# Kernel optimization log

Hardware: AMD Instinct MI355X
Metric: run time of the kernel (lower is better)

Reference implementation:

```python
import jax, jax.numpy as jnp
import numpy as np

N_NODES = 50000; N_INTRA = 800000; N_INTER = 400000; N_IEDGE = 600000
N_GRAPHS = 128; F_IN = 54; DIM = 128; N_GNN = 3; DIM_MLP = 128
DEV_VDW_COEFF = 0.2; EPS_LO = 0.0178; EPS_HI = 0.2
VDW_N_SHORT = 10.0; VDW_N_LONG = 6.0
RANGE_LO = 0.5; RANGE_HI = 5.0
HBOND_CUT = (-0.7, 0.0); METAL_CUT = (-0.7, 0.0); HYDRO_CUT = (0.5, 1.5)


def _lin(key, fi, fo):
    return jax.random.normal(key, (fi, fo), jnp.float32) / np.float32(np.sqrt(fi))


def setup_inputs():
    key = jax.random.key(0)
    ks = iter(jax.random.split(key, 48))
    nk = lambda: next(ks)
    inp = {}
    inp['x'] = jax.random.normal(nk(), (N_NODES, F_IN), jnp.float32)
    inp['pos'] = jax.random.uniform(nk(), (N_NODES, 3), jnp.float32, 0.0, 20.0)
    inp['vdw_radii'] = jax.random.uniform(nk(), (N_NODES,), jnp.float32, 1.0, 2.0)
    inp['rotor'] = jax.random.randint(nk(), (N_GRAPHS, 1), 0, 20).astype(jnp.float32)
    inp['edge_index'] = jax.random.randint(nk(), (2, N_INTRA), 0, N_NODES)
    inp['edge_index_c'] = jax.random.randint(nk(), (2, N_INTER), 0, N_NODES)
    inp['edge_index_i'] = jax.random.randint(nk(), (2, N_IEDGE), 0, N_NODES)
    inp['batch'] = jnp.sort(jax.random.randint(nk(), (N_NODES,), 0, N_GRAPHS))
    for name, p in (('is_metal', 0.02), ('is_h_donor', 0.15), ('is_h_acceptor', 0.2), ('is_hydrophobic', 0.4)):
        inp[name] = jax.random.bernoulli(nk(), p, (N_NODES,))
    inp['embed_W'] = _lin(nk(), F_IN, DIM)
    inp['gat_W'] = jax.random.normal(nk(), (N_GNN, DIM, DIM), jnp.float32) / np.float32(np.sqrt(DIM))
    inp['gat_Wb'] = jnp.zeros((N_GNN, DIM), jnp.float32)
    inp['gat_A'] = 0.1 * jax.random.normal(nk(), (N_GNN, DIM, DIM), jnp.float32) / np.float32(np.sqrt(DIM))
    inp['gat_gate_w'] = jax.random.normal(nk(), (N_GNN, 2 * DIM, 1), jnp.float32) / np.float32(np.sqrt(2 * DIM))
    inp['gat_gate_b'] = jnp.zeros((N_GNN, 1), jnp.float32)
    inp['inter_W'] = jax.random.normal(nk(), (N_GNN, DIM, DIM), jnp.float32) / np.float32(np.sqrt(DIM))
    inp['inter_Wb'] = jnp.zeros((N_GNN, DIM), jnp.float32)
    inp['inter_gate_w'] = jax.random.normal(nk(), (N_GNN, 2 * DIM, 1), jnp.float32) / np.float32(np.sqrt(2 * DIM))
    inp['inter_gate_b'] = jnp.zeros((N_GNN, 1), jnp.float32)
    inp['eps_w1'] = _lin(nk(), 2 * DIM, DIM_MLP); inp['eps_b1'] = jnp.zeros((DIM_MLP,), jnp.float32)
    inp['eps_w2'] = _lin(nk(), DIM_MLP, 1); inp['eps_b2'] = jnp.zeros((1,), jnp.float32)
    inp['dvdw_w1'] = _lin(nk(), 2 * DIM, DIM_MLP); inp['dvdw_b1'] = jnp.zeros((DIM_MLP,), jnp.float32)
    inp['dvdw_w2'] = _lin(nk(), DIM_MLP, 1); inp['dvdw_b2'] = jnp.zeros((1,), jnp.float32)
    inp['hbond_coeff'] = jnp.array([1.0], jnp.float32)
    inp['hydrophobic_coeff'] = jnp.array([0.5], jnp.float32)
    inp['rotor_coeff'] = jnp.array([0.5], jnp.float32)
    return inp


def _gated_gat(x, src, dst, W, Wb, A, gw, gb):
    n = x.shape[0]
    h = x @ W + Wb                                   # [N, D]
    logits = jnp.sum((h @ A)[dst] * h[src], axis=-1)  # per-edge attention logit
    mx = jax.ops.segment_max(logits, dst, num_segments=n)
    mx = jnp.where(jnp.isfinite(mx), mx, 0.0)
    ex = jnp.exp(logits - mx[dst])
    den = jax.ops.segment_sum(ex, dst, num_segments=n)
    alpha = ex / (den[dst] + 1e-16)                  # segment softmax over incoming edges
    h_prime = jax.nn.relu(jax.ops.segment_sum(alpha[:, None] * h[src], dst, num_segments=n))
    z = jax.nn.sigmoid(jnp.concatenate([x, h_prime], -1) @ gw + gb)
    return z * x + (1.0 - z) * h_prime


def _interaction(x, src, dst, W, Wb, gw, gb):
    n = x.shape[0]
    m = jax.ops.segment_sum(jax.nn.relu(x[src] @ W + Wb), dst, num_segments=n)
    z = jax.nn.sigmoid(jnp.concatenate([x, m], -1) @ gw + gb)
    return z * x + (1.0 - z) * m


def _lj(D, R, eps, n_short, n_long):
    dr = jnp.maximum(D / R, 0.5)  # numerical clamp mirroring PIGNet's distance clamp
    n = jnp.where(dr < 1.0, n_short, n_long)
    return eps * (dr ** (-2.0 * n) - 2.0 * dr ** (-n))


def _linear_potential(D, R, minima, c_short, c_long):
    frac = jnp.clip(((D - R) - c_long) / (c_short - c_long), 0.0, 1.0)
    return minima * frac


def _forward(x, pos, vdw_radii, rotor, embed_W, gat_W, gat_Wb, gat_A, gat_gate_w, gat_gate_b,
             inter_W, inter_Wb, inter_gate_w, inter_gate_b,
             eps_w1, eps_b1, eps_w2, eps_b2, dvdw_w1, dvdw_b1, dvdw_w2, dvdw_b2,
             hbond_coeff, hydrophobic_coeff, rotor_coeff,
             edge_index, edge_index_c, edge_index_i, batch,
             is_metal, is_h_donor, is_h_acceptor, is_hydrophobic):
    h = x @ embed_W
    for l in range(N_GNN):
        h = _gated_gat(h, edge_index[0], edge_index[1], gat_W[l], gat_Wb[l], gat_A[l], gat_gate_w[l], gat_gate_b[l])
    for l in range(N_GNN):
        h = _interaction(h, edge_index_c[0], edge_index_c[1], inter_W[l], inter_Wb[l], inter_gate_w[l], inter_gate_b[l])
    i, j = edge_index_i[0], edge_index_i[1]
    diff = pos[i] - pos[j]
    D = jnp.sqrt(jnp.sum(diff * diff, axis=-1) + 1e-10)           # [E]
    rmask = ((D >= RANGE_LO) & (D <= RANGE_HI)).astype(h.dtype)
    x_cat = jnp.concatenate([h[i], h[j]], axis=-1)                # [E, 2*DIM]
    dvdw = jnp.tanh(jax.nn.relu(x_cat @ dvdw_w1 + dvdw_b1) @ dvdw_w2 + dvdw_b2)[:, 0]
    dvdw = dvdw * DEV_VDW_COEFF * rmask
    R = vdw_radii[i] + vdw_radii[j] + dvdw
    eps = jax.nn.sigmoid(jax.nn.relu(x_cat @ eps_w1 + eps_b1) @ eps_w2 + eps_b2)[:, 0]
    eps = eps * (EPS_HI - EPS_LO) + EPS_LO
    min_hb = -hbond_coeff ** 2
    min_hp = -hydrophobic_coeff ** 2
    e = jnp.stack([
        _lj(D, R, eps, VDW_N_SHORT, VDW_N_LONG),
        _linear_potential(D, R, min_hb, *HBOND_CUT),
        _linear_potential(D, R, min_hb, *METAL_CUT),
        _linear_potential(D, R, min_hp, *HYDRO_CUT),
    ])                                                            # [4, E]
    no_metal = ~(is_metal[i] | is_metal[j])
    masks = jnp.stack([
        no_metal,
        ((is_h_donor[i] & is_h_acceptor[j]) | (is_h_acceptor[i] & is_h_donor[j])) & no_metal,
        (is_metal[i] & is_h_acceptor[j]) | (is_h_acceptor[i] & is_metal[j]),
        is_hydrophobic[i] & is_hydrophobic[j] & no_metal,
    ]).astype(e.dtype)
    e = e * masks * rmask
    energies = jax.ops.segment_sum(e.T, batch[i], num_segments=N_GRAPHS)  # [G, 4]
    penalty = 1.0 + rotor_coeff ** 2 * rotor                               # [G, 1]
    return energies / penalty, dvdw


def reference(x, pos, vdw_radii, rotor, edge_index, edge_index_c, edge_index_i, batch,
              is_metal, is_h_donor, is_h_acceptor, is_hydrophobic,
              embed_W, gat_W, gat_Wb, gat_A, gat_gate_w, gat_gate_b,
              inter_W, inter_Wb, inter_gate_w, inter_gate_b,
              eps_w1, eps_b1, eps_w2, eps_b2, dvdw_w1, dvdw_b1, dvdw_w2, dvdw_b2,
              hbond_coeff, hydrophobic_coeff, rotor_coeff):
    return _forward(x, pos, vdw_radii, rotor, embed_W, gat_W, gat_Wb, gat_A, gat_gate_w, gat_gate_b,
                    inter_W, inter_Wb, inter_gate_w, inter_gate_b,
                    eps_w1, eps_b1, eps_w2, eps_b2, dvdw_w1, dvdw_b1, dvdw_w2, dvdw_b2,
                    hbond_coeff, hydrophobic_coeff, rotor_coeff,
                    edge_index, edge_index_c, edge_index_i, batch,
                    is_metal, is_h_donor, is_h_acceptor, is_hydrophobic)
```

## Files before the change

### kernel.cpp

```cpp
#include <hip/hip_runtime.h>
#include <math.h>

#define NN 50000
#define EA 800000
#define EC 400000
#define EIN 600000
#define NG 128
#define FIN 54

#define DEV_VDW 0.2f
#define EPS_LO_ 0.0178f
#define EPS_HI_ 0.2f

typedef unsigned int uint;
typedef unsigned short ushort;
typedef unsigned long long ull;
typedef __attribute__((ext_vector_type(8))) short bf16x8;
typedef __attribute__((ext_vector_type(4))) float f32x4;

__device__ __forceinline__ ushort f2bf(float f){
  uint x = __float_as_uint(f);
  uint r = x + 0x7fffu + ((x >> 16) & 1u);
  return (ushort)(r >> 16);
}
__device__ __forceinline__ uint f2bf2(float a, float b){
  return (uint)f2bf(a) | ((uint)f2bf(b) << 16);
}
__device__ __forceinline__ void decode8(uint4 u, float* f){
  f[0] = __uint_as_float(u.x << 16); f[1] = __uint_as_float(u.x & 0xffff0000u);
  f[2] = __uint_as_float(u.y << 16); f[3] = __uint_as_float(u.y & 0xffff0000u);
  f[4] = __uint_as_float(u.z << 16); f[5] = __uint_as_float(u.z & 0xffff0000u);
  f[6] = __uint_as_float(u.w << 16); f[7] = __uint_as_float(u.w & 0xffff0000u);
}

__global__ void k_rank(const int* __restrict__ dstA, const int* __restrict__ dstC,
                       const int* __restrict__ dstI,
                       int* __restrict__ cntA, int* __restrict__ cntC, int* __restrict__ cntI,
                       int* __restrict__ rnkA, int* __restrict__ rnkC, int* __restrict__ rnkI){
  int b = blockIdx.x;
  const int* dst; int* cnt; int* rnk; int E; int bid; int nb;
  if (b < 1024){ dst = dstA; cnt = cntA; rnk = rnkA; E = EA;  bid = b;        nb = 1024; }
  else if (b < 1536){ dst = dstC; cnt = cntC; rnk = rnkC; E = EC;  bid = b - 1024; nb = 512; }
  else { dst = dstI; cnt = cntI; rnk = rnkI; E = EIN; bid = b - 1536; nb = 1024; }
  for (int i = bid * 256 + threadIdx.x; i < E; i += nb * 256)
    rnk[i] = atomicAdd(&cnt[dst[i]], 1);
}

__global__ void k_scan3(const int* __restrict__ cntA, int* __restrict__ offA,
                        const int* __restrict__ cntC, int* __restrict__ offC,
                        const int* __restrict__ cntI, int* __restrict__ offI){
  const int* cnt = (blockIdx.x == 0) ? cntA : (blockIdx.x == 1) ? cntC : cntI;
  int* off = (blockIdx.x == 0) ? offA : (blockIdx.x == 1) ? offC : offI;
  int n = NN;
  __shared__ int wsums[16];
  __shared__ int run_s;
  int tid = threadIdx.x;
  int lane = tid & 63, w = tid >> 6;
  if (tid == 0) run_s = 0;
  __syncthreads();
  for (int base = 0; base < n; base += 1024){
    int run = run_s;
    int i = base + tid;
    int v = (i < n) ? cnt[i] : 0;
    int s = v;
    #pragma unroll
    for (int o = 1; o < 64; o <<= 1){ int t = __shfl_up(s, o, 64); if (lane >= o) s += t; }
    if (lane == 63) wsums[w] = s;
    __syncthreads();
    if (w == 0 && lane < 16){
      int t = wsums[lane];
      #pragma unroll
      for (int o = 1; o < 16; o <<= 1){ int u = __shfl_up(t, o, 64); if (lane >= o) t += u; }
      wsums[lane] = t;
    }
    __syncthreads();
    int woff = (w == 0) ? 0 : wsums[w - 1];
    int excl = run + woff + (s - v);
    if (i < n) off[i] = excl;
    int tot = wsums[15];
    __syncthreads();
    if (tid == 0) run_s = run + tot;
    __syncthreads();
  }
  if (threadIdx.x == 0) off[n] = run_s;
}

__global__ void k_place(const int* __restrict__ eiA, const int* __restrict__ eiC,
                        const int* __restrict__ eiI,
                        const int* __restrict__ offA, const int* __restrict__ rnkA, int* __restrict__ srcA,
                        const int* __restrict__ offC, const int* __restrict__ rnkC, int* __restrict__ srcC,
                        const int* __restrict__ offI, const int* __restrict__ rnkI, ull* __restrict__ jeI){
  int b = blockIdx.x;
  if (b < 1024){
    for (int i = b * 256 + threadIdx.x; i < EA; i += 1024 * 256){
      int d = eiA[EA + i];
      __builtin_nontemporal_store(eiA[i], &srcA[offA[d] + rnkA[i]]);
    }
  } else if (b < 1536){
    int bid = b - 1024;
    for (int i = bid * 256 + threadIdx.x; i < EC; i += 512 * 256){
      int d = eiC[EC + i];
      __builtin_nontemporal_store(eiC[i], &srcC[offC[d] + rnkC[i]]);
    }
  } else {
    int bid = b - 1536;
    for (int i = bid * 256 + threadIdx.x; i < EIN; i += 1024 * 256){
      int key = eiI[i];
      ull v = ((ull)(uint)i << 32) | (uint)eiI[EIN + i];
      __builtin_nontemporal_store(v, &jeI[offI[key] + rnkI[i]]);
    }
  }
}

__global__ void k_nodeinfo(const float* __restrict__ POS, const float* __restrict__ RAD,
                           const int* __restrict__ Mmet, const int* __restrict__ Mdon,
                           const int* __restrict__ Macc, const int* __restrict__ Mhyd,
                           const int* __restrict__ BATCH,
                           float4* __restrict__ PRAD, uint* __restrict__ MB){
  int n = blockIdx.x * 256 + threadIdx.x;
  if (n < NN){
    PRAD[n] = make_float4(POS[3*n], POS[3*n+1], POS[3*n+2], RAD[n]);
    uint m = (Mmet[n] ? 1u : 0u) | (Mdon[n] ? 2u : 0u) | (Macc[n] ? 4u : 0u) |
             (Mhyd[n] ? 8u : 0u) | ((uint)BATCH[n] << 8);
    MB[n] = m;
  }
}

__global__ __launch_bounds__(256) void k_prepw(const float* __restrict__ gatW, const float* __restrict__ gatA,
                        const float* __restrict__ intW, const float* __restrict__ dw1,
                        const float* __restrict__ ew1,
                        const float* __restrict__ gatWb, const float* __restrict__ intWb,
                        const float* __restrict__ db1, const float* __restrict__ eb1,
                        uint* __restrict__ Wt, float* __restrict__ BIASALL){
  __shared__ ushort L[128 * 132];
  int m = blockIdx.x;
  int tid = threadIdx.x;
  if (m == 13){
    for (int idx = tid; idx < 13 * 128; idx += 256){
      int slot = idx >> 7, c = idx & 127;
      if (slot >= 3 && slot < 6) continue;
      float v = 0.f;
      if (slot < 3) v = gatWb[slot * 128 + c];
      else if (slot < 9) v = intWb[(slot - 6) * 128 + c];
      else if (slot == 9) v = db1[c];
      else if (slot == 11) v = eb1[c];
      BIASALL[idx] = v;
    }
    return;
  }
  if (m >= 3 && m < 6){
    int l = m - 3;
    const float* Wf  = gatW + l * 16384;
    const float* Af  = gatA + l * 16384;
    const float* Wbf = gatWb + l * 128;
    for (int idx = tid; idx < 16384; idx += 256){
      int k = idx >> 7, n = idx & 127;
      L[k * 132 + n] = f2bf(Af[idx]);
    }
    __syncthreads();
    int r = tid >> 1, ch = tid & 1;
    float accv[64];
    #pragma unroll
    for (int c = 0; c < 64; ++c) accv[c] = 0.f;
    float accb = 0.f;
    int bc = tid & 127;
    for (int mm = 0; mm < 128; ++mm){
      float wv = Wf[r * 128 + mm];
      const uint* Lr32 = (const uint*)&L[mm * 132 + ch * 64];
      #pragma unroll
      for (int c2 = 0; c2 < 32; ++c2){
        uint u = Lr32[c2];
        accv[2 * c2]     += wv * __uint_as_float(u << 16);
        accv[2 * c2 + 1] += wv * __uint_as_float(u & 0xffff0000u);
      }
      accb += Wbf[mm] * __uint_as_float((uint)L[mm * 132 + bc] << 16);
    }
    __syncthreads();
    #pragma unroll
    for (int c = 0; c < 64; ++c) L[r * 132 + ch * 64 + c] = f2bf(accv[c]);
    if (tid < 128) BIASALL[(3 + l) * 128 + tid] = accb;
    __syncthreads();
    int n = tid & 127, half = tid >> 7;
    uint* outp = Wt + (size_t)m * 8192 + n * 64 + half * 32;
    #pragma unroll
    for (int kk2 = 0; kk2 < 32; ++kk2){
      int k = half * 64 + 2 * kk2;
      uint u = (uint)L[k * 132 + n] | ((uint)L[(k + 1) * 132 + n] << 16);
      outp[kk2] = u;
    }
    return;
  }
  const float* src = (m < 3)  ? gatW + m * 16384 :
                     (m < 9)  ? intW + (m - 6) * 16384 :
                     (m < 11) ? dw1 + (m - 9) * 16384 :
                                ew1 + (m - 11) * 16384;
  for (int idx = tid; idx < 16384; idx += 256){
    int k = idx >> 7, n = idx & 127;
    L[k * 132 + n] = f2bf(src[idx]);
  }
  __syncthreads();
  int n = tid & 127, half = tid >> 7;
  uint* outp = Wt + (size_t)m * 8192 + n * 64 + half * 32;
  #pragma unroll
  for (int kk2 = 0; kk2 < 32; ++kk2){
    int k = half * 64 + 2 * kk2;
    uint u = (uint)L[k * 132 + n] | ((uint)L[(k + 1) * 132 + n] << 16);
    outp[kk2] = u;
  }
}

__global__ void k_embed(const float* __restrict__ X, const float* __restrict__ W,
                        uint* __restrict__ Hh){
  __shared__ float Wls[FIN * 128];
  int tid = threadIdx.x;
  for (int i = tid; i < FIN * 128; i += 128) Wls[i] = W[i];
  __syncthreads();
  for (int row = blockIdx.x; row < NN; row += gridDim.x){
    const float* xr = X + row * FIN;
    float acc = 0.f;
    #pragma unroll
    for (int k = 0; k < FIN; ++k) acc += xr[k] * Wls[k * 128 + tid];
    ((ushort*)Hh)[(size_t)row * 128 + tid] = f2bf(acc);
  }
}

template<bool RELU>
__global__ __launch_bounds__(256) void k_gemm_mfma(const uint* __restrict__ Ah,
        const uint* __restrict__ Bt0, size_t strideB,
        const float* __restrict__ bias0, size_t strideBias,
        uint* __restrict__ C0, size_t strideC, int N){
  const uint* Bt = Bt0 + (size_t)blockIdx.y * strideB;
  const float* bias = bias0 + (size_t)blockIdx.y * strideBias;
  uint* Cout = C0 + (size_t)blockIdx.y * strideC;
  int tid = threadIdx.x;
  int lane = tid & 63;
  int wv = tid >> 6;
  int row0 = blockIdx.x * 128 + wv * 32;
  int l15 = lane & 15, lg = lane >> 4;
  int ra0 = row0 + l15, ra1 = row0 + 16 + l15;
  const uint* pa0 = Ah + (size_t)(ra0 < N ? ra0 : 0) * 64 + lg * 4;
  const uint* pa1 = Ah + (size_t)(ra1 < N ? ra1 : 0) * 64 + lg * 4;
  const uint* pb  = Bt + (size_t)l15 * 64 + lg * 4;
  f32x4 acc[2][8] = {};
  #pragma unroll
  for (int c = 0; c < 4; ++c){
    bf16x8 a0 = *(const bf16x8*)(pa0 + c * 16);
    bf16x8 a1 = *(const bf16x8*)(pa1 + c * 16);
    #pragma unroll
    for (int ct = 0; ct < 8; ++ct){
      bf16x8 b = *(const bf16x8*)(pb + ct * 1024 + c * 16);
      acc[0][ct] = __builtin_amdgcn_mfma_f32_16x16x32_bf16(a0, b, acc[0][ct], 0, 0, 0);
      acc[1][ct] = __builtin_amdgcn_mfma_f32_16x16x32_bf16(a1, b, acc[1][ct], 0, 0, 0);
    }
  }
  #pragma unroll
  for (int ct = 0; ct < 8; ++ct){
    int col = ct * 16 + l15;
    float bv = bias[col];
    #pragma unroll
    for (int rt = 0; rt < 2; ++rt){
      int rbase = row0 + rt * 16 + lg * 4;
      f32x4 a4 = acc[rt][ct];
      #pragma unroll
      for (int r = 0; r < 4; ++r){
        int row = rbase + r;
        if (row < N){
          float t = a4[r] + bv;
          if (RELU) t = fmaxf(t, 0.f);
          ((ushort*)Cout)[(size_t)row * 128 + col] = f2bf(t);
        }
      }
    }
  }
}

__global__ __launch_bounds__(256) void k_gat(uint* __restrict__ Hh,
                      const uint* __restrict__ HWh, const uint* __restrict__ HAh,
                      const int* __restrict__ off, const int* __restrict__ srcs,
                      const float* __restrict__ GW, const float* __restrict__ GB){
  int tid = threadIdx.x;
  int sub = tid & 15;
  int n = blockIdx.x * 16 + (tid >> 4);
  if (n >= NN) return;
  uint4 au = *(const uint4*)(HAh + (size_t)n * 64 + sub * 4);
  float a[8]; decode8(au, a);
  int e0 = off[n], deg = off[n + 1] - e0;
  float m = -INFINITY, den = 0.f;
  float acc[8] = {};
  uint4 w0v = {}, w1v = {}, w2v = {};
  if (deg > 0) w0v = *(const uint4*)(HWh + (size_t)srcs[e0] * 64 + sub * 4);
  if (deg > 1) w1v = *(const uint4*)(HWh + (size_t)srcs[e0 + 1] * 64 + sub * 4);
  if (deg > 2) w2v = *(const uint4*)(HWh + (size_t)srcs[e0 + 2] * 64 + sub * 4);
  for (int t = 0; t < deg; ++t){
    uint4 wn = {};
    if (t + 3 < deg) wn = *(const uint4*)(HWh + (size_t)srcs[e0 + t + 3] * 64 + sub * 4);
    float w[8]; decode8(w0v, w);
    float p = a[0]*w[0] + a[1]*w[1] + a[2]*w[2] + a[3]*w[3]
            + a[4]*w[4] + a[5]*w[5] + a[6]*w[6] + a[7]*w[7];
    #pragma unroll
    for (int o = 8; o; o >>= 1) p += __shfl_xor(p, o, 64);
    float mn = fmaxf(m, p);
    float cf = __expf(m - mn);
    float ex = __expf(p - mn);
    den = den * cf + ex;
    #pragma unroll
    for (int q = 0; q < 8; ++q) acc[q] = acc[q] * cf + ex * w[q];
    m = mn;
    w0v = w1v; w1v = w2v; w2v = wn;
  }
  float inv = 1.f / (den + 1e-16f);
  float hp[8];
  #pragma unroll
  for (int q = 0; q < 8; ++q) hp[q] = fmaxf(acc[q] * inv, 0.f);
  uint4 xu = *(const uint4*)(Hh + (size_t)n * 64 + sub * 4);
  float x[8]; decode8(xu, x);
  float gx[8], gh[8];
  *(float4*)&gx[0] = *(const float4*)(GW + sub * 8);
  *(float4*)&gx[4] = *(const float4*)(GW + sub * 8 + 4);
  *(float4*)&gh[0] = *(const float4*)(GW + 128 + sub * 8);
  *(float4*)&gh[4] = *(const float4*)(GW + 128 + sub * 8 + 4);
  float g = 0.f;
  #pragma unroll
  for (int q = 0; q < 8; ++q) g += x[q] * gx[q] + hp[q] * gh[q];
  #pragma unroll
  for (int o = 8; o; o >>= 1) g += __shfl_xor(g, o, 64);
  g += GB[0];
  float z = 1.f / (1.f + __expf(-g));
  #pragma unroll
  for (int q = 0; q < 8; ++q) x[q] = z * x[q] + (1.f - z) * hp[q];
  uint4 hw;
  hw.x = f2bf2(x[0], x[1]); hw.y = f2bf2(x[2], x[3]);
  hw.z = f2bf2(x[4], x[5]); hw.w = f2bf2(x[6], x[7]);
  *(uint4*)(Hh + (size_t)n * 64 + sub * 4) = hw;
}

__global__ __launch_bounds__(256) void k_inter(uint* __restrict__ Hh,
                        const uint* __restrict__ Th,
                        const int* __restrict__ off, const int* __restrict__ srcs,
                        const float* __restrict__ GW, const float* __restrict__ GB){
  int tid = threadIdx.x;
  int sub = tid & 15;
  int n = blockIdx.x * 16 + (tid >> 4);
  if (n >= NN) return;
  int e0 = off[n], deg = off[n + 1] - e0;
  float acc[8] = {};
  uint4 w0v = {}, w1v = {}, w2v = {};
  if (deg > 0) w0v = *(const uint4*)(Th + (size_t)srcs[e0] * 64 + sub * 4);
  if (deg > 1) w1v = *(const uint4*)(Th + (size_t)srcs[e0 + 1] * 64 + sub * 4);
  if (deg > 2) w2v = *(const uint4*)(Th + (size_t)srcs[e0 + 2] * 64 + sub * 4);
  for (int t = 0; t < deg; ++t){
    uint4 wn = {};
    if (t + 3 < deg) wn = *(const uint4*)(Th + (size_t)srcs[e0 + t + 3] * 64 + sub * 4);
    float w[8]; decode8(w0v, w);
    #pragma unroll
    for (int q = 0; q < 8; ++q) acc[q] += w[q];
    w0v = w1v; w1v = w2v; w2v = wn;
  }
  uint4 xu = *(const uint4*)(Hh + (size_t)n * 64 + sub * 4);
  float x[8]; decode8(xu, x);
  float gx[8], gh[8];
  *(float4*)&gx[0] = *(const float4*)(GW + sub * 8);
  *(float4*)&gx[4] = *(const float4*)(GW + sub * 8 + 4);
  *(float4*)&gh[0] = *(const float4*)(GW + 128 + sub * 8);
  *(float4*)&gh[4] = *(const float4*)(GW + 128 + sub * 8 + 4);
  float g = 0.f;
  #pragma unroll
  for (int q = 0; q < 8; ++q) g += x[q] * gx[q] + acc[q] * gh[q];
  #pragma unroll
  for (int o = 8; o; o >>= 1) g += __shfl_xor(g, o, 64);
  g += GB[0];
  float z = 1.f / (1.f + __expf(-g));
  #pragma unroll
  for (int q = 0; q < 8; ++q) x[q] = z * x[q] + (1.f - z) * acc[q];
  uint4 hw;
  hw.x = f2bf2(x[0], x[1]); hw.y = f2bf2(x[2], x[3]);
  hw.z = f2bf2(x[4], x[5]); hw.w = f2bf2(x[6], x[7]);
  *(uint4*)(Hh + (size_t)n * 64 + sub * 4) = hw;
}

__global__ __launch_bounds__(256) void k_edges(
    const int* __restrict__ offI, const ull* __restrict__ jeI,
    const float4* __restrict__ PRAD, const uint* __restrict__ MB,
    const uint* __restrict__ Pd, const uint* __restrict__ Qd,
    const uint* __restrict__ Pe, const uint* __restrict__ Qe,
    const float* __restrict__ w2d, const float* __restrict__ b2d,
    const float* __restrict__ w2e, const float* __restrict__ b2e,
    const float* __restrict__ hbc, const float* __restrict__ hpc,
    float* __restrict__ geng, float* __restrict__ outdv){
  int tid = threadIdx.x;
  int sub = tid & 15;
  int n = blockIdx.x * 16 + (tid >> 4);
  if (n >= NN) return;
  int e0 = offI[n], deg = offI[n + 1] - e0;
  if (deg == 0) return;
  float wdv[8], wev[8];
  *(float4*)&wdv[0] = *(const float4*)(w2d + sub * 8);
  *(float4*)&wdv[4] = *(const float4*)(w2d + sub * 8 + 4);
  *(float4*)&wev[0] = *(const float4*)(w2e + sub * 8);
  *(float4*)&wev[4] = *(const float4*)(w2e + sub * 8 + 4);
  float bd = b2d[0], be = b2e[0];
  float minhb = -hbc[0] * hbc[0], minhp = -hpc[0] * hpc[0];
  uint4 pdu = *(const uint4*)(Pd + (size_t)n * 64 + sub * 4);
  uint4 peu = *(const uint4*)(Pe + (size_t)n * 64 + sub * 4);
  float pdf[8], pef[8];
  decode8(pdu, pdf); decode8(peu, pef);
  float4 pri = PRAD[n];
  uint mbi = MB[n];
  float E0 = 0.f, E1 = 0.f, E2 = 0.f, E3 = 0.f;

  ull je0 = jeI[e0];
  int j0 = (int)(uint)je0;
  uint4 qd0 = *(const uint4*)(Qd + (size_t)j0 * 64 + sub * 4);
  uint4 qe0 = *(const uint4*)(Qe + (size_t)j0 * 64 + sub * 4);
  float4 prj0 = PRAD[j0];
  uint mbj0 = MB[j0];

  for (int t = 0; t < deg; ++t){
    ull je1 = 0; uint4 qd1 = {}, qe1 = {}; float4 prj1 = {}; uint mbj1 = 0;
    if (t + 1 < deg){
      je1 = jeI[e0 + t + 1];
      int j1 = (int)(uint)je1;
      qd1 = *(const uint4*)(Qd + (size_t)j1 * 64 + sub * 4);
      qe1 = *(const uint4*)(Qe + (size_t)j1 * 64 + sub * 4);
      prj1 = PRAD[j1]; mbj1 = MB[j1];
    }
    float qdf[8], qef[8];
    decode8(qd0, qdf); decode8(qe0, qef);
    float sd = 0.f, se = 0.f;
    #pragma unroll
    for (int q = 0; q < 8; ++q){
      sd += fmaxf(pdf[q] + qdf[q], 0.f) * wdv[q];
      se += fmaxf(pef[q] + qef[q], 0.f) * wev[q];
    }
    #pragma unroll
    for (int o = 8; o; o >>= 1){
      sd += __shfl_xor(sd, o, 64);
      se += __shfl_xor(se, o, 64);
    }
    sd += bd; se += be;
    float dx = pri.x - prj0.x, dy = pri.y - prj0.y, dz = pri.z - prj0.z;
    float D = sqrtf(dx * dx + dy * dy + dz * dz + 1e-10f);
    float rmask = (D >= 0.5f && D <= 5.0f) ? 1.f : 0.f;
    float ex2 = __expf(2.f * fminf(sd, 15.f));
    float th = __fdividef(ex2 - 1.f, ex2 + 1.f);
    float dvdw = th * DEV_VDW * rmask;
    float eps = __fdividef(1.f, 1.f + __expf(-se)) * (EPS_HI_ - EPS_LO_) + EPS_LO_;
    float R = pri.w + prj0.w + dvdw;
    float dr = fmaxf(__fdividef(D, R), 0.5f);
    float nn2 = (dr < 1.f) ? 10.f : 6.f;
    float tp = __expf(-nn2 * __logf(dr));
    float ev = eps * (tp * tp - 2.f * tp);
    float dmr = D - R;
    float f1 = fminf(fmaxf(dmr * (-1.f / 0.7f), 0.f), 1.f);
    float f3 = fminf(fmaxf(1.5f - dmr, 0.f), 1.f);
    bool metI = mbi & 1, metJ = mbj0 & 1;
    bool donI = mbi & 2, donJ = mbj0 & 2;
    bool accI = mbi & 4, accJ = mbj0 & 4;
    bool hyI  = mbi & 8, hyJ  = mbj0 & 8;
    bool nm = !(metI || metJ);
    if (sub == 0) __builtin_nontemporal_store(dvdw, &outdv[(int)(je0 >> 32)]);
    E0 += nm ? ev * rmask : 0.f;
    E1 += (((donI && accJ) || (accI && donJ)) && nm) ? minhb * f1 * rmask : 0.f;
    E2 += ((metI && accJ) || (accI && metJ)) ? minhb * f1 * rmask : 0.f;
    E3 += (hyI && hyJ && nm) ? minhp * f3 * rmask : 0.f;
    je0 = je1; qd0 = qd1; qe0 = qe1; prj0 = prj1; mbj0 = mbj1;
  }
  if (sub == 0){
    float* part = geng + (size_t)(blockIdx.x & 7) * (NG * 4);
    int g = (int)(mbi >> 8) * 4;
    atomicAdd(&part[g + 0], E0);
    atomicAdd(&part[g + 1], E1);
    atomicAdd(&part[g + 2], E2);
    atomicAdd(&part[g + 3], E3);
  }
}

__global__ void k_final(const float* __restrict__ geng, const float* __restrict__ rotor,
                        const float* __restrict__ rc, float* __restrict__ out){
  int t = blockIdx.x * blockDim.x + threadIdx.x;
  if (t < NG * 4){
    int g = t >> 2;
    float s = 0.f;
    #pragma unroll
    for (int p = 0; p < 8; ++p) s += geng[p * NG * 4 + t];
    float pen = 1.f + rc[0] * rc[0] * rotor[g];
    out[t] = s / pen;
  }
}

extern "C" void kernel_launch(void* const* d_in, const int* in_sizes, int n_in,
                              void* d_out, int out_size, void* d_ws, size_t ws_size,
                              hipStream_t stream){
  (void)in_sizes; (void)n_in; (void)out_size; (void)ws_size;
  const float* X    = (const float*)d_in[0];
  const float* POS  = (const float*)d_in[1];
  const float* RAD  = (const float*)d_in[2];
  const float* ROT  = (const float*)d_in[3];
  const int* EIa    = (const int*)d_in[4];
  const int* EIc    = (const int*)d_in[5];
  const int* EIi    = (const int*)d_in[6];
  const int* BATCH  = (const int*)d_in[7];
  const int* Mmet = (const int*)d_in[8];
  const int* Mdon = (const int*)d_in[9];
  const int* Macc = (const int*)d_in[10];
  const int* Mhyd = (const int*)d_in[11];
  const float* embW  = (const float*)d_in[12];
  const float* gatW  = (const float*)d_in[13];
  const float* gatWb = (const float*)d_in[14];
  const float* gatA  = (const float*)d_in[15];
  const float* gatGw = (const float*)d_in[16];
  const float* gatGb = (const float*)d_in[17];
  const float* intW  = (const float*)d_in[18];
  const float* intWb = (const float*)d_in[19];
  const float* intGw = (const float*)d_in[20];
  const float* intGb = (const float*)d_in[21];
  const float* ew1 = (const float*)d_in[22];
  const float* eb1 = (const float*)d_in[23];
  const float* ew2 = (const float*)d_in[24];
  const float* eb2 = (const float*)d_in[25];
  const float* dw1 = (const float*)d_in[26];
  const float* db1 = (const float*)d_in[27];
  const float* dw2 = (const float*)d_in[28];
  const float* db2 = (const float*)d_in[29];
  const float* hbc = (const float*)d_in[30];
  const float* hpc = (const float*)d_in[31];
  const float* rcc = (const float*)d_in[32];
  float* out = (float*)d_out;

  char* w = (char*)d_ws;
  uint* Hh   = (uint*)w;  w += (size_t)NN * 64 * 4;
  uint* BAh  = (uint*)w;  w += (size_t)NN * 64 * 4;
  uint* BBh  = (uint*)w;  w += (size_t)NN * 64 * 4;
  uint* Peh  = (uint*)w;  w += (size_t)NN * 64 * 4;
  uint* Qeh  = (uint*)w;  w += (size_t)NN * 64 * 4;
  uint* WT   = (uint*)w;  w += (size_t)13 * 8192 * 4;
  float* BIASALL = (float*)w; w += (size_t)13 * 128 * 4;
  float4* PRAD = (float4*)w; w += (size_t)NN * 16;
  uint* MBb  = (uint*)w;  w += (size_t)NN * 4;
  float* GENG = (float*)w; w += (size_t)8 * 512 * 4;
  int* cntA = (int*)w; w += (size_t)NN * 4;
  int* offA = (int*)w; w += (size_t)(NN + 1) * 4;
  int* srcA = (int*)w; w += (size_t)EA * 4;
  int* rnkA = (int*)w; w += (size_t)EA * 4;
  int* cntC = (int*)w; w += (size_t)NN * 4;
  int* offC = (int*)w; w += (size_t)(NN + 1) * 4;
  int* srcC = (int*)w; w += (size_t)EC * 4;
  int* rnkC = (int*)w; w += (size_t)EC * 4;
  int* cntI = (int*)w; w += (size_t)NN * 4;
  int* offI = (int*)w; w += (size_t)(NN + 1) * 4;
  int* rnkI = (int*)w; w += (size_t)EIN * 4;
  ull* jeI  = (ull*)w; w += (size_t)EIN * 8;
  uint* Th  = BAh;
  uint* Pdh = BAh;
  uint* Qdh = BBh;

  hipMemsetAsync(cntA, 0, (size_t)NN * 4, stream);
  hipMemsetAsync(cntC, 0, (size_t)NN * 4, stream);
  hipMemsetAsync(cntI, 0, (size_t)NN * 4, stream);
  hipMemsetAsync(GENG, 0, (size_t)8 * 512 * 4, stream);

  k_rank<<<2560, 256, 0, stream>>>(EIa + EA, EIc + EC, EIi, cntA, cntC, cntI, rnkA, rnkC, rnkI);
  k_scan3<<<3, 1024, 0, stream>>>(cntA, offA, cntC, offC, cntI, offI);
  k_place<<<2560, 256, 0, stream>>>(EIa, EIc, EIi, offA, rnkA, srcA, offC, rnkC, srcC, offI, rnkI, jeI);

  k_prepw<<<14, 256, 0, stream>>>(gatW, gatA, intW, dw1, ew1, gatWb, intWb, db1, eb1, WT, BIASALL);
  k_nodeinfo<<<(NN + 255) / 256, 256, 0, stream>>>(POS, RAD, Mmet, Mdon, Macc, Mhyd, BATCH, PRAD, MBb);
  k_embed<<<2048, 128, 0, stream>>>(X, embW, Hh);

  int gg = (NN + 127) / 128;
  int nodeGrid = (NN + 15) / 16;
  for (int l = 0; l < 3; ++l){
    k_gemm_mfma<false><<<dim3(gg, 2), 256, 0, stream>>>(Hh, WT + (size_t)l * 8192, (size_t)3 * 8192,
                                                        BIASALL + l * 128, (size_t)3 * 128,
                                                        BAh, (size_t)NN * 64, NN);
    k_gat<<<nodeGrid, 256, 0, stream>>>(Hh, BAh, BBh, offA, srcA, gatGw + l * 256, gatGb + l);
  }
  for (int l = 0; l < 3; ++l){
    k_gemm_mfma<true><<<dim3(gg, 1), 256, 0, stream>>>(Hh, WT + (size_t)(6 + l) * 8192, 0,
                                                       BIASALL + (6 + l) * 128, 0, Th, 0, NN);
    k_inter<<<nodeGrid, 256, 0, stream>>>(Hh, Th, offC, srcC, intGw + l * 256, intGb + l);
  }
  k_gemm_mfma<false><<<dim3(gg, 4), 256, 0, stream>>>(Hh, WT + (size_t)9 * 8192, (size_t)8192,
                                                      BIASALL + 9 * 128, (size_t)128,
                                                      BAh, (size_t)NN * 64, NN);

  k_edges<<<nodeGrid, 256, 0, stream>>>(offI, jeI, PRAD, MBb, Pdh, Qdh, Peh, Qeh,
                                        dw2, db2, ew2, eb2, hbc, hpc,
                                        GENG, out + 512);
  k_final<<<2, 256, 0, stream>>>(GENG, ROT, rcc, out);
}
```

Before: 889.0 us.

## Use atomic-cursor CSR placement, fuse setup kernels, balance edge work evenly

Edge bucketing now counts without storing ranks and takes slots from an atomic cursor copied from the scan, which removes the rank arrays. Weight prep, node info and the embedding are merged into one launch, and the four memsets become one. The online softmax in the GAT kernel uses a single exponential per edge instead of two. The interaction-edge kernel splits edges evenly across groups instead of one group per node, and flushes per-graph partial sums whenever the graph changes. The cost is extra gathers of the i-side rows per edge and more atomics, and slot order within a node is no longer deterministic.

```diff
diff --git a/kernel.cpp b/kernel.cpp
--- a/kernel.cpp
+++ b/kernel.cpp
@@ -33,24 +33,23 @@
   f[6] = __uint_as_float(u.w << 16); f[7] = __uint_as_float(u.w & 0xffff0000u);
 }
 
-__global__ void k_rank(const int* __restrict__ dstA, const int* __restrict__ dstC,
-                       const int* __restrict__ dstI,
-                       int* __restrict__ cntA, int* __restrict__ cntC, int* __restrict__ cntI,
-                       int* __restrict__ rnkA, int* __restrict__ rnkC, int* __restrict__ rnkI){
+__global__ void k_count(const int* __restrict__ dstA, const int* __restrict__ dstC,
+                        const int* __restrict__ dstI,
+                        int* __restrict__ cntA, int* __restrict__ cntC, int* __restrict__ cntI){
   int b = blockIdx.x;
-  const int* dst; int* cnt; int* rnk; int E; int bid; int nb;
-  if (b < 1024){ dst = dstA; cnt = cntA; rnk = rnkA; E = EA;  bid = b;        nb = 1024; }
-  else if (b < 1536){ dst = dstC; cnt = cntC; rnk = rnkC; E = EC;  bid = b - 1024; nb = 512; }
-  else { dst = dstI; cnt = cntI; rnk = rnkI; E = EIN; bid = b - 1536; nb = 1024; }
-  for (int i = bid * 256 + threadIdx.x; i < E; i += nb * 256)
-    rnk[i] = atomicAdd(&cnt[dst[i]], 1);
-}
-
-__global__ void k_scan3(const int* __restrict__ cntA, int* __restrict__ offA,
-                        const int* __restrict__ cntC, int* __restrict__ offC,
-                        const int* __restrict__ cntI, int* __restrict__ offI){
+  const int* dst; int* cnt; int E; int bid; int nb;
+  if (b < 1024){ dst = dstA; cnt = cntA; E = EA;  bid = b;        nb = 1024; }
+  else if (b < 1536){ dst = dstC; cnt = cntC; E = EC;  bid = b - 1024; nb = 512; }
+  else { dst = dstI; cnt = cntI; E = EIN; bid = b - 1536; nb = 1024; }
+  for (int i = bid * 256 + threadIdx.x; i < E; i += nb * 256) atomicAdd(&cnt[dst[i]], 1);
+}
+
+__global__ void k_scan3(const int* __restrict__ cntA, int* __restrict__ offA, int* __restrict__ curA,
+                        const int* __restrict__ cntC, int* __restrict__ offC, int* __restrict__ curC,
+                        const int* __restrict__ cntI, int* __restrict__ offI, int* __restrict__ curI){
   const int* cnt = (blockIdx.x == 0) ? cntA : (blockIdx.x == 1) ? cntC : cntI;
   int* off = (blockIdx.x == 0) ? offA : (blockIdx.x == 1) ? offC : offI;
+  int* cur = (blockIdx.x == 0) ? curA : (blockIdx.x == 1) ? curC : curI;
   int n = NN;
   __shared__ int wsums[16];
   __shared__ int run_s;
@@ -76,7 +75,7 @@
     __syncthreads();
     int woff = (w == 0) ? 0 : wsums[w - 1];
     int excl = run + woff + (s - v);
-    if (i < n) off[i] = excl;
+    if (i < n){ off[i] = excl; cur[i] = excl; }
     int tot = wsums[15];
     __syncthreads();
     if (tid == 0) run_s = run + tot;
@@ -87,54 +86,78 @@
 
 __global__ void k_place(const int* __restrict__ eiA, const int* __restrict__ eiC,
                         const int* __restrict__ eiI,
-                        const int* __restrict__ offA, const int* __restrict__ rnkA, int* __restrict__ srcA,
-                        const int* __restrict__ offC, const int* __restrict__ rnkC, int* __restrict__ srcC,
-                        const int* __restrict__ offI, const int* __restrict__ rnkI, ull* __restrict__ jeI){
+                        int* __restrict__ curA, int* __restrict__ srcA,
+                        int* __restrict__ curC, int* __restrict__ srcC,
+                        int* __restrict__ curI, ull* __restrict__ jeI, int* __restrict__ iI){
   int b = blockIdx.x;
   if (b < 1024){
     for (int i = b * 256 + threadIdx.x; i < EA; i += 1024 * 256){
       int d = eiA[EA + i];
-      __builtin_nontemporal_store(eiA[i], &srcA[offA[d] + rnkA[i]]);
+      int slot = atomicAdd(&curA[d], 1);
+      __builtin_nontemporal_store(eiA[i], &srcA[slot]);
     }
   } else if (b < 1536){
     int bid = b - 1024;
     for (int i = bid * 256 + threadIdx.x; i < EC; i += 512 * 256){
       int d = eiC[EC + i];
-      __builtin_nontemporal_store(eiC[i], &srcC[offC[d] + rnkC[i]]);
+      int slot = atomicAdd(&curC[d], 1);
+      __builtin_nontemporal_store(eiC[i], &srcC[slot]);
     }
   } else {
     int bid = b - 1536;
     for (int i = bid * 256 + threadIdx.x; i < EIN; i += 1024 * 256){
       int key = eiI[i];
+      int slot = atomicAdd(&curI[key], 1);
       ull v = ((ull)(uint)i << 32) | (uint)eiI[EIN + i];
-      __builtin_nontemporal_store(v, &jeI[offI[key] + rnkI[i]]);
-    }
-  }
-}
-
-__global__ void k_nodeinfo(const float* __restrict__ POS, const float* __restrict__ RAD,
-                           const int* __restrict__ Mmet, const int* __restrict__ Mdon,
-                           const int* __restrict__ Macc, const int* __restrict__ Mhyd,
-                           const int* __restrict__ BATCH,
-                           float4* __restrict__ PRAD, uint* __restrict__ MB){
-  int n = blockIdx.x * 256 + threadIdx.x;
-  if (n < NN){
-    PRAD[n] = make_float4(POS[3*n], POS[3*n+1], POS[3*n+2], RAD[n]);
-    uint m = (Mmet[n] ? 1u : 0u) | (Mdon[n] ? 2u : 0u) | (Macc[n] ? 4u : 0u) |
-             (Mhyd[n] ? 8u : 0u) | ((uint)BATCH[n] << 8);
-    MB[n] = m;
-  }
-}
-
-__global__ __launch_bounds__(256) void k_prepw(const float* __restrict__ gatW, const float* __restrict__ gatA,
+      __builtin_nontemporal_store(v, &jeI[slot]);
+      __builtin_nontemporal_store(key, &iI[slot]);
+    }
+  }
+}
+
+__global__ __launch_bounds__(256) void k_misc(
+                        const float* __restrict__ gatW, const float* __restrict__ gatA,
                         const float* __restrict__ intW, const float* __restrict__ dw1,
                         const float* __restrict__ ew1,
                         const float* __restrict__ gatWb, const float* __restrict__ intWb,
                         const float* __restrict__ db1, const float* __restrict__ eb1,
-                        uint* __restrict__ Wt, float* __restrict__ BIASALL){
-  __shared__ ushort L[128 * 132];
-  int m = blockIdx.x;
+                        uint* __restrict__ Wt, float* __restrict__ BIASALL,
+                        const float* __restrict__ POS, const float* __restrict__ RAD,
+                        const int* __restrict__ Mmet, const int* __restrict__ Mdon,
+                        const int* __restrict__ Macc, const int* __restrict__ Mhyd,
+                        const int* __restrict__ BATCH,
+                        float4* __restrict__ PRAD, uint* __restrict__ MB,
+                        const float* __restrict__ X, const float* __restrict__ embW,
+                        uint* __restrict__ Hh){
+  __shared__ char SMEM[33792];
+  int b = blockIdx.x;
   int tid = threadIdx.x;
+  if (b >= 210){
+    float* Wls = (float*)SMEM;
+    for (int i = tid; i < FIN * 128; i += 256) Wls[i] = embW[i];
+    __syncthreads();
+    int col = tid & 127, rh = tid >> 7;
+    for (int row = (b - 210) * 2 + rh; row < NN; row += 4096){
+      const float* xr = X + row * FIN;
+      float acc = 0.f;
+      #pragma unroll
+      for (int k = 0; k < FIN; ++k) acc += xr[k] * Wls[k * 128 + col];
+      ((ushort*)Hh)[(size_t)row * 128 + col] = f2bf(acc);
+    }
+    return;
+  }
+  if (b >= 14){
+    int n = (b - 14) * 256 + tid;
+    if (n < NN){
+      PRAD[n] = make_float4(POS[3*n], POS[3*n+1], POS[3*n+2], RAD[n]);
+      uint m = (Mmet[n] ? 1u : 0u) | (Mdon[n] ? 2u : 0u) | (Macc[n] ? 4u : 0u) |
+               (Mhyd[n] ? 8u : 0u) | ((uint)BATCH[n] << 8);
+      MB[n] = m;
+    }
+    return;
+  }
+  int m = b;
+  ushort* L = (ushort*)SMEM;
   if (m == 13){
     for (int idx = tid; idx < 13 * 128; idx += 256){
       int slot = idx >> 7, c = idx & 127;
@@ -206,21 +229,6 @@
     int k = half * 64 + 2 * kk2;
     uint u = (uint)L[k * 132 + n] | ((uint)L[(k + 1) * 132 + n] << 16);
     outp[kk2] = u;
-  }
-}
-
-__global__ void k_embed(const float* __restrict__ X, const float* __restrict__ W,
-                        uint* __restrict__ Hh){
-  __shared__ float Wls[FIN * 128];
-  int tid = threadIdx.x;
-  for (int i = tid; i < FIN * 128; i += 128) Wls[i] = W[i];
-  __syncthreads();
-  for (int row = blockIdx.x; row < NN; row += gridDim.x){
-    const float* xr = X + row * FIN;
-    float acc = 0.f;
-    #pragma unroll
-    for (int k = 0; k < FIN; ++k) acc += xr[k] * Wls[k * 128 + tid];
-    ((ushort*)Hh)[(size_t)row * 128 + tid] = f2bf(acc);
   }
 }
 
@@ -299,13 +307,15 @@
             + a[4]*w[4] + a[5]*w[5] + a[6]*w[6] + a[7]*w[7];
     #pragma unroll
     for (int o = 8; o; o >>= 1) p += __shfl_xor(p, o, 64);
-    float mn = fmaxf(m, p);
-    float cf = __expf(m - mn);
-    float ex = __expf(p - mn);
+    float d = p - m;
+    float eB = __expf(-fabsf(d));
+    bool up = d > 0.f;
+    float cf = up ? eB : 1.f;
+    float ex = up ? 1.f : eB;
     den = den * cf + ex;
     #pragma unroll
     for (int q = 0; q < 8; ++q) acc[q] = acc[q] * cf + ex * w[q];
-    m = mn;
+    if (up) m = p;
     w0v = w1v; w1v = w2v; w2v = wn;
   }
   float inv = 1.f / (den + 1e-16f);
@@ -379,7 +389,7 @@
 }
 
 __global__ __launch_bounds__(256) void k_edges(
-    const int* __restrict__ offI, const ull* __restrict__ jeI,
+    const int* __restrict__ iI, const ull* __restrict__ jeI,
     const float4* __restrict__ PRAD, const uint* __restrict__ MB,
     const uint* __restrict__ Pd, const uint* __restrict__ Qd,
     const uint* __restrict__ Pe, const uint* __restrict__ Qe,
@@ -389,10 +399,11 @@
     float* __restrict__ geng, float* __restrict__ outdv){
   int tid = threadIdx.x;
   int sub = tid & 15;
-  int n = blockIdx.x * 16 + (tid >> 4);
-  if (n >= NN) return;
-  int e0 = offI[n], deg = offI[n + 1] - e0;
-  if (deg == 0) return;
+  int gid = blockIdx.x * 16 + (tid >> 4);
+  int ngrp = gridDim.x * 16;
+  int e0 = (int)((long)EIN * gid / ngrp);
+  int e1 = (int)((long)EIN * (gid + 1) / ngrp);
+  if (e0 >= e1) return;
   float wdv[8], wev[8];
   *(float4*)&wdv[0] = *(const float4*)(w2d + sub * 8);
   *(float4*)&wdv[4] = *(const float4*)(w2d + sub * 8 + 4);
@@ -400,32 +411,35 @@
   *(float4*)&wev[4] = *(const float4*)(w2e + sub * 8 + 4);
   float bd = b2d[0], be = b2e[0];
   float minhb = -hbc[0] * hbc[0], minhp = -hpc[0] * hpc[0];
-  uint4 pdu = *(const uint4*)(Pd + (size_t)n * 64 + sub * 4);
-  uint4 peu = *(const uint4*)(Pe + (size_t)n * 64 + sub * 4);
-  float pdf[8], pef[8];
-  decode8(pdu, pdf); decode8(peu, pef);
-  float4 pri = PRAD[n];
-  uint mbi = MB[n];
   float E0 = 0.f, E1 = 0.f, E2 = 0.f, E3 = 0.f;
-
-  ull je0 = jeI[e0];
-  int j0 = (int)(uint)je0;
-  uint4 qd0 = *(const uint4*)(Qd + (size_t)j0 * 64 + sub * 4);
-  uint4 qe0 = *(const uint4*)(Qe + (size_t)j0 * 64 + sub * 4);
-  float4 prj0 = PRAD[j0];
-  uint mbj0 = MB[j0];
-
-  for (int t = 0; t < deg; ++t){
-    ull je1 = 0; uint4 qd1 = {}, qe1 = {}; float4 prj1 = {}; uint mbj1 = 0;
-    if (t + 1 < deg){
-      je1 = jeI[e0 + t + 1];
-      int j1 = (int)(uint)je1;
-      qd1 = *(const uint4*)(Qd + (size_t)j1 * 64 + sub * 4);
-      qe1 = *(const uint4*)(Qe + (size_t)j1 * 64 + sub * 4);
-      prj1 = PRAD[j1]; mbj1 = MB[j1];
-    }
-    float qdf[8], qef[8];
-    decode8(qd0, qdf); decode8(qe0, qef);
+  int gcur = -1;
+  float* part = geng + (size_t)(blockIdx.x & 7) * (NG * 4);
+
+  int ia = iI[e0];
+  ull je = jeI[e0];
+  int ja = (int)(uint)je;
+  uint4 pd0 = *(const uint4*)(Pd + (size_t)ia * 64 + sub * 4);
+  uint4 pe0 = *(const uint4*)(Pe + (size_t)ia * 64 + sub * 4);
+  uint4 qd0 = *(const uint4*)(Qd + (size_t)ja * 64 + sub * 4);
+  uint4 qe0 = *(const uint4*)(Qe + (size_t)ja * 64 + sub * 4);
+  float4 pri = PRAD[ia], prj = PRAD[ja];
+  uint mbi = MB[ia], mbj = MB[ja];
+
+  for (int e = e0; e < e1; ++e){
+    ull jeN = 0; uint4 pdN = {}, peN = {}, qdN = {}, qeN = {};
+    float4 priN = {}, prjN = {}; uint mbiN = 0, mbjN = 0;
+    if (e + 1 < e1){
+      int iN = iI[e + 1];
+      jeN = jeI[e + 1];
+      int jN = (int)(uint)jeN;
+      pdN = *(const uint4*)(Pd + (size_t)iN * 64 + sub * 4);
+      peN = *(const uint4*)(Pe + (size_t)iN * 64 + sub * 4);
+      qdN = *(const uint4*)(Qd + (size_t)jN * 64 + sub * 4);
+      qeN = *(const uint4*)(Qe + (size_t)jN * 64 + sub * 4);
+      priN = PRAD[iN]; prjN = PRAD[jN]; mbiN = MB[iN]; mbjN = MB[jN];
+    }
+    float pdf[8], qdf[8], pef[8], qef[8];
+    decode8(pd0, pdf); decode8(qd0, qdf); decode8(pe0, pef); decode8(qe0, qef);
     float sd = 0.f, se = 0.f;
     #pragma unroll
     for (int q = 0; q < 8; ++q){
@@ -438,14 +452,14 @@
       se += __shfl_xor(se, o, 64);
     }
     sd += bd; se += be;
-    float dx = pri.x - prj0.x, dy = pri.y - prj0.y, dz = pri.z - prj0.z;
+    float dx = pri.x - prj.x, dy = pri.y - prj.y, dz = pri.z - prj.z;
     float D = sqrtf(dx * dx + dy * dy + dz * dz + 1e-10f);
     float rmask = (D >= 0.5f && D <= 5.0f) ? 1.f : 0.f;
     float ex2 = __expf(2.f * fminf(sd, 15.f));
     float th = __fdividef(ex2 - 1.f, ex2 + 1.f);
     float dvdw = th * DEV_VDW * rmask;
     float eps = __fdividef(1.f, 1.f + __expf(-se)) * (EPS_HI_ - EPS_LO_) + EPS_LO_;
-    float R = pri.w + prj0.w + dvdw;
+    float R = pri.w + prj.w + dvdw;
     float dr = fmaxf(__fdividef(D, R), 0.5f);
     float nn2 = (dr < 1.f) ? 10.f : 6.f;
     float tp = __expf(-nn2 * __logf(dr));
@@ -453,25 +467,35 @@
     float dmr = D - R;
     float f1 = fminf(fmaxf(dmr * (-1.f / 0.7f), 0.f), 1.f);
     float f3 = fminf(fmaxf(1.5f - dmr, 0.f), 1.f);
-    bool metI = mbi & 1, metJ = mbj0 & 1;
-    bool donI = mbi & 2, donJ = mbj0 & 2;
-    bool accI = mbi & 4, accJ = mbj0 & 4;
-    bool hyI  = mbi & 8, hyJ  = mbj0 & 8;
+    bool metI = mbi & 1, metJ = mbj & 1;
+    bool donI = mbi & 2, donJ = mbj & 2;
+    bool accI = mbi & 4, accJ = mbj & 4;
+    bool hyI  = mbi & 8, hyJ  = mbj & 8;
     bool nm = !(metI || metJ);
-    if (sub == 0) __builtin_nontemporal_store(dvdw, &outdv[(int)(je0 >> 32)]);
+    if (sub == 0) __builtin_nontemporal_store(dvdw, &outdv[(int)(je >> 32)]);
+    int g = (int)(mbi >> 8);
+    if (g != gcur){
+      if (sub == 0 && gcur >= 0){
+        atomicAdd(&part[gcur * 4 + 0], E0);
+        atomicAdd(&part[gcur * 4 + 1], E1);
+        atomicAdd(&part[gcur * 4 + 2], E2);
+        atomicAdd(&part[gcur * 4 + 3], E3);
+      }
+      E0 = E1 = E2 = E3 = 0.f;
+      gcur = g;
+    }
     E0 += nm ? ev * rmask : 0.f;
     E1 += (((donI && accJ) || (accI && donJ)) && nm) ? minhb * f1 * rmask : 0.f;
     E2 += ((metI && accJ) || (accI && metJ)) ? minhb * f1 * rmask : 0.f;
     E3 += (hyI && hyJ && nm) ? minhp * f3 * rmask : 0.f;
-    je0 = je1; qd0 = qd1; qe0 = qe1; prj0 = prj1; mbj0 = mbj1;
-  }
-  if (sub == 0){
-    float* part = geng + (size_t)(blockIdx.x & 7) * (NG * 4);
-    int g = (int)(mbi >> 8) * 4;
-    atomicAdd(&part[g + 0], E0);
-    atomicAdd(&part[g + 1], E1);
-    atomicAdd(&part[g + 2], E2);
-    atomicAdd(&part[g + 3], E3);
+    je = jeN; pd0 = pdN; pe0 = peN; qd0 = qdN; qe0 = qeN;
+    pri = priN; prj = prjN; mbi = mbiN; mbj = mbjN;
+  }
+  if (sub == 0 && gcur >= 0){
+    atomicAdd(&part[gcur * 4 + 0], E0);
+    atomicAdd(&part[gcur * 4 + 1], E1);
+    atomicAdd(&part[gcur * 4 + 2], E2);
+    atomicAdd(&part[gcur * 4 + 3], E3);
   }
 }
 
@@ -537,35 +561,34 @@
   float* BIASALL = (float*)w; w += (size_t)13 * 128 * 4;
   float4* PRAD = (float4*)w; w += (size_t)NN * 16;
   uint* MBb  = (uint*)w;  w += (size_t)NN * 4;
+  int* cntA = (int*)w; w += (size_t)NN * 4;
+  int* cntC = (int*)w; w += (size_t)NN * 4;
+  int* cntI = (int*)w; w += (size_t)NN * 4;
   float* GENG = (float*)w; w += (size_t)8 * 512 * 4;
-  int* cntA = (int*)w; w += (size_t)NN * 4;
+  size_t zero_bytes = (size_t)3 * NN * 4 + (size_t)8 * 512 * 4;
   int* offA = (int*)w; w += (size_t)(NN + 1) * 4;
+  int* curA = (int*)w; w += (size_t)NN * 4;
   int* srcA = (int*)w; w += (size_t)EA * 4;
-  int* rnkA = (int*)w; w += (size_t)EA * 4;
-  int* cntC = (int*)w; w += (size_t)NN * 4;
   int* offC = (int*)w; w += (size_t)(NN + 1) * 4;
+  int* curC = (int*)w; w += (size_t)NN * 4;
   int* srcC = (int*)w; w += (size_t)EC * 4;
-  int* rnkC = (int*)w; w += (size_t)EC * 4;
-  int* cntI = (int*)w; w += (size_t)NN * 4;
   int* offI = (int*)w; w += (size_t)(NN + 1) * 4;
-  int* rnkI = (int*)w; w += (size_t)EIN * 4;
+  int* curI = (int*)w; w += (size_t)NN * 4;
   ull* jeI  = (ull*)w; w += (size_t)EIN * 8;
+  int* iI   = (int*)w; w += (size_t)EIN * 4;
   uint* Th  = BAh;
   uint* Pdh = BAh;
   uint* Qdh = BBh;
 
-  hipMemsetAsync(cntA, 0, (size_t)NN * 4, stream);
-  hipMemsetAsync(cntC, 0, (size_t)NN * 4, stream);
-  hipMemsetAsync(cntI, 0, (size_t)NN * 4, stream);
-  hipMemsetAsync(GENG, 0, (size_t)8 * 512 * 4, stream);
-
-  k_rank<<<2560, 256, 0, stream>>>(EIa + EA, EIc + EC, EIi, cntA, cntC, cntI, rnkA, rnkC, rnkI);
-  k_scan3<<<3, 1024, 0, stream>>>(cntA, offA, cntC, offC, cntI, offI);
-  k_place<<<2560, 256, 0, stream>>>(EIa, EIc, EIi, offA, rnkA, srcA, offC, rnkC, srcC, offI, rnkI, jeI);
-
-  k_prepw<<<14, 256, 0, stream>>>(gatW, gatA, intW, dw1, ew1, gatWb, intWb, db1, eb1, WT, BIASALL);
-  k_nodeinfo<<<(NN + 255) / 256, 256, 0, stream>>>(POS, RAD, Mmet, Mdon, Macc, Mhyd, BATCH, PRAD, MBb);
-  k_embed<<<2048, 128, 0, stream>>>(X, embW, Hh);
+  hipMemsetAsync(cntA, 0, zero_bytes, stream);
+
+  k_count<<<2560, 256, 0, stream>>>(EIa + EA, EIc + EC, EIi, cntA, cntC, cntI);
+  k_scan3<<<3, 1024, 0, stream>>>(cntA, offA, curA, cntC, offC, curC, cntI, offI, curI);
+  k_place<<<2560, 256, 0, stream>>>(EIa, EIc, EIi, curA, srcA, curC, srcC, curI, jeI, iI);
+
+  k_misc<<<2258, 256, 0, stream>>>(gatW, gatA, intW, dw1, ew1, gatWb, intWb, db1, eb1,
+                                   WT, BIASALL, POS, RAD, Mmet, Mdon, Macc, Mhyd, BATCH,
+                                   PRAD, MBb, X, embW, Hh);
 
   int gg = (NN + 127) / 128;
   int nodeGrid = (NN + 15) / 16;
@@ -584,7 +607,7 @@
                                                       BIASALL + 9 * 128, (size_t)128,
                                                       BAh, (size_t)NN * 64, NN);
 
-  k_edges<<<nodeGrid, 256, 0, stream>>>(offI, jeI, PRAD, MBb, Pdh, Qdh, Peh, Qeh,
+  k_edges<<<nodeGrid, 256, 0, stream>>>(iI, jeI, PRAD, MBb, Pdh, Qdh, Peh, Qeh,
                                         dw2, db2, ew2, eb2, hbc, hpc,
                                         GENG, out + 512);
   k_final<<<2, 256, 0, stream>>>(GENG, ROT, rcc, out);
```

Result: slower. 1.017 ms (+14.4%).
